# Kernel tuning notes

Hardware: AMD Instinct MI355X
Metric: run time of the kernel (lower is better)

The kernel has to match this reference:

```python
import jax, jax.numpy as jnp
import numpy as np

ROPE_BASE = 10000.0


def _apply_rope(q, k, start_pos):
    # q, k: (B, T, H, D) with half-split (LLaMA-style) rotation
    B, T, H, D = q.shape
    half = D // 2
    inv_freq = 1.0 / (ROPE_BASE ** (jnp.arange(0, half, dtype=jnp.float32) / half))
    pos = (start_pos + jnp.arange(T)).astype(jnp.float32)
    ang = pos[:, None] * inv_freq[None, :]          # (T, half)
    cos = jnp.cos(ang)[None, :, None, :]            # (1, T, 1, half)
    sin = jnp.sin(ang)[None, :, None, :]

    def rot(t):
        t1, t2 = t[..., :half], t[..., half:]
        return jnp.concatenate([t1 * cos - t2 * sin, t1 * sin + t2 * cos], axis=-1)

    return rot(q), rot(k)


def setup_inputs() -> dict:
    key = jax.random.key(0)
    k1, k2, k3 = jax.random.split(key, 3)
    B, T, C = 2, 2048, 2048
    x = jax.random.normal(k1, (B, T, C), dtype=jnp.float32)
    # torch Linear weights: (out_features, in_features), scaled like default init
    Wqkv = jax.random.normal(k2, (3 * C, C), dtype=jnp.float32) * (C ** -0.5)
    Wproj = jax.random.normal(k3, (C, C), dtype=jnp.float32) * (C ** -0.5)
    return {"x": x, "Wqkv": Wqkv, "Wproj": Wproj, "start_pos": 0}


def reference(x, Wqkv, Wproj, start_pos):
    B, T, C = x.shape
    H = 16
    D = C // H
    scale = D ** -0.5

    qkv = x @ Wqkv.T                                 # (B, T, 3C)
    q, k, v = jnp.split(qkv, 3, axis=-1)
    q = q.reshape(B, T, H, D)
    k = k.reshape(B, T, H, D)
    v = v.reshape(B, T, H, D)
    q, k = _apply_rope(q, k, start_pos)

    att = jnp.einsum("bthd,bshd->bhts", q, k) * scale   # (B, H, T, T)
    causal = jnp.tril(jnp.ones((T, T), dtype=bool))
    att = jnp.where(causal[None, None], att, -jnp.inf)
    att = jax.nn.softmax(att, axis=-1)
    out = jnp.einsum("bhts,bshd->bthd", att, v)          # (B, T, H, D)
    out = out.reshape(B, T, C)
    return out @ Wproj.T
```

## Files before the change

kernel.cpp:

```cpp
#include <hip/hip_runtime.h>
#include <hip/hip_bf16.h>
#include <stdint.h>
#include <math.h>

#define B_    2
#define T_    2048
#define C_    2048
#define H_    16
#define D_    128
#define NQKV  6144
#define BT_   4096

typedef __attribute__((ext_vector_type(8)))  short short8;
typedef __attribute__((ext_vector_type(4)))  short short4_;
typedef __attribute__((ext_vector_type(4)))  float float4_;
typedef __attribute__((ext_vector_type(16))) float f32x16;

__device__ __forceinline__ unsigned short f2bf(float f) {
  union { float f; unsigned int u; } v; v.f = f;
  unsigned int u = v.u;
  return (unsigned short)((u + 0x7FFFu + ((u >> 16) & 1u)) >> 16);
}
__device__ __forceinline__ float bf2f(unsigned short u) {
  union { unsigned int i; float f; } v; v.i = ((unsigned int)u) << 16;
  return v.f;
}
__device__ __forceinline__ void pk2(short4_& dst, int idx2, float a, float b) {
  union { __hip_bfloat162 h2; struct { short x, y; } s; } u;
  u.h2 = __float22bfloat162_rn(make_float2(a, b));
  dst[idx2 * 2]     = u.s.x;
  dst[idx2 * 2 + 1] = u.s.y;
}

__device__ __forceinline__ void async_cp16(const unsigned short* g, unsigned short* l) {
  __builtin_amdgcn_global_load_lds((__attribute__((address_space(1))) void*)g,
                                   (__attribute__((address_space(3))) void*)l,
                                   16, 0, 0);
}

__global__ __launch_bounds__(256) void cvt_all(const float* __restrict__ x,
                                               const float* __restrict__ wqkv,
                                               const float* __restrict__ wproj,
                                               const int* __restrict__ sp_ptr,
                                               unsigned short* __restrict__ out,
                                               float* __restrict__ ct,
                                               float* __restrict__ st) {
  if (blockIdx.x >= 12288) {
    int j = (blockIdx.x - 12288) * 256 + threadIdx.x;
    int d = j & 63;
    const float L2F = -0.20762050593046013f;
    float fr = exp2f((float)d * L2F);
    float ang = (float)(sp_ptr[0] + (j >> 6)) * fr;
    ct[j] = cosf(ang);
    st[j] = sinf(ang);
    return;
  }
  int i = (blockIdx.x * 256 + threadIdx.x) * 8;
  const float* src; int off;
  if (i < 8388608)       { src = x;     off = i; }
  else if (i < 20971520) { src = wqkv;  off = i - 8388608; }
  else                   { src = wproj; off = i - 20971520; }
  const float4_* p = (const float4_*)(src + off);
  float4_ a = p[0], b = p[1];
  short8 o;
  o[0] = (short)f2bf(a[0]); o[1] = (short)f2bf(a[1]);
  o[2] = (short)f2bf(a[2]); o[3] = (short)f2bf(a[3]);
  o[4] = (short)f2bf(b[0]); o[5] = (short)f2bf(b[1]);
  o[6] = (short)f2bf(b[2]); o[7] = (short)f2bf(b[3]);
  *(short8*)(out + i) = o;
}

template <bool F32OUT>
__global__ __launch_bounds__(256) void gemm_bt(const unsigned short* __restrict__ A,
                                               const unsigned short* __restrict__ Bm,
                                               void* __restrict__ Cout,
                                               int M, int N, int K) {
  __shared__ __align__(16) unsigned short As[128 * 64];
  __shared__ __align__(16) unsigned short Bs[128 * 64];
  const int tid  = threadIdx.x;
  const int lane = tid & 63;
  const int col16 = lane & 15, quad = lane >> 4;
  const int wave = tid >> 6;
  const int wm = wave >> 1, wn = wave & 1;
  const int m0 = blockIdx.y * 128, n0 = blockIdx.x * 128;

  float4_ acc[4][4] = {};

  #pragma unroll 1
  for (int k0 = 0; k0 < K; k0 += 64) {
    __syncthreads();
    #pragma unroll
    for (int i = 0; i < 4; ++i) {
      int P   = i * 256 + tid;
      int row = P >> 3;
      int kc  = (P & 7) ^ (row & 7);
      async_cp16(A  + (size_t)(m0 + row) * K + k0 + kc * 8, As + P * 8);
      async_cp16(Bm + (size_t)(n0 + row) * K + k0 + kc * 8, Bs + P * 8);
    }
    __syncthreads();
    #pragma unroll
    for (int ks = 0; ks < 2; ++ks) {
      short8 af[4], bf[4];
      #pragma unroll
      for (int i = 0; i < 4; ++i) {
        int ra = wm * 64 + i * 16 + col16;
        int ca = ((ks * 4 + quad) ^ (ra & 7)) * 8;
        af[i] = *(const short8*)(As + ra * 64 + ca);
        int rb = wn * 64 + i * 16 + col16;
        int cb = ((ks * 4 + quad) ^ (rb & 7)) * 8;
        bf[i] = *(const short8*)(Bs + rb * 64 + cb);
      }
      #pragma unroll
      for (int i = 0; i < 4; ++i)
        #pragma unroll
        for (int j = 0; j < 4; ++j)
          acc[i][j] = __builtin_amdgcn_mfma_f32_16x16x32_bf16(af[i], bf[j], acc[i][j], 0, 0, 0);
    }
  }

  #pragma unroll
  for (int i = 0; i < 4; ++i) {
    int mg = m0 + wm * 64 + i * 16 + quad * 4;
    #pragma unroll
    for (int j = 0; j < 4; ++j) {
      int ng = n0 + wn * 64 + j * 16 + col16;
      #pragma unroll
      for (int r = 0; r < 4; ++r) {
        if constexpr (F32OUT)
          ((float*)Cout)[(size_t)(mg + r) * N + ng] = acc[i][j][r];
        else
          ((unsigned short*)Cout)[(size_t)(mg + r) * N + ng] = f2bf(acc[i][j][r]);
      }
    }
  }
}

__global__ __launch_bounds__(256) void gemm_qkv(const unsigned short* __restrict__ A,
                                                const unsigned short* __restrict__ Bm,
                                                const float* __restrict__ ct,
                                                const float* __restrict__ st,
                                                unsigned short* __restrict__ q_r,
                                                unsigned short* __restrict__ k_r,
                                                unsigned short* __restrict__ v_t) {
  __shared__ __align__(16) unsigned short S[16384];
  unsigned short* As = S;
  unsigned short* Bs = S + 8192;
  const int tid  = threadIdx.x;
  const int lane = tid & 63;
  const int col16 = lane & 15, quad = lane >> 4;
  const int wave = tid >> 6;
  const int wm = wave >> 1, wn = wave & 1;
  const int m0 = blockIdx.y * 128, n0 = blockIdx.x * 128;

  float4_ acc[4][4] = {};

  #pragma unroll 1
  for (int k0 = 0; k0 < C_; k0 += 64) {
    __syncthreads();
    #pragma unroll
    for (int i = 0; i < 4; ++i) {
      int P   = i * 256 + tid;
      int row = P >> 3;
      int kc  = (P & 7) ^ (row & 7);
      async_cp16(A  + (size_t)(m0 + row) * C_ + k0 + kc * 8, As + P * 8);
      async_cp16(Bm + (size_t)(n0 + row) * C_ + k0 + kc * 8, Bs + P * 8);
    }
    __syncthreads();
    #pragma unroll
    for (int ks = 0; ks < 2; ++ks) {
      short8 af[4], bf[4];
      #pragma unroll
      for (int i = 0; i < 4; ++i) {
        int ra = wm * 64 + i * 16 + col16;
        int ca = ((ks * 4 + quad) ^ (ra & 7)) * 8;
        af[i] = *(const short8*)(As + ra * 64 + ca);
        int rb = wn * 32 + (i & 1) * 16 + (i >> 1) * 64 + col16;
        int cb = ((ks * 4 + quad) ^ (rb & 7)) * 8;
        bf[i] = *(const short8*)(Bs + rb * 64 + cb);
      }
      #pragma unroll
      for (int i = 0; i < 4; ++i)
        #pragma unroll
        for (int j = 0; j < 4; ++j)
          acc[i][j] = __builtin_amdgcn_mfma_f32_16x16x32_bf16(af[i], bf[j], acc[i][j], 0, 0, 0);
    }
  }

  const int region = n0 >> 11;
  const int h   = (n0 & 2047) >> 7;
  const int b   = m0 >> 11;
  const int t0l = m0 & 2047;
  const int bh  = b * H_ + h;

  if (region < 2) {
    unsigned short* dst = region ? k_r : q_r;
    const float scl = region ? 1.0f : 0.1275174117f;
    #pragma unroll
    for (int i = 0; i < 4; ++i) {
      int tl = t0l + wm * 64 + i * 16 + quad * 4;
      #pragma unroll
      for (int jl = 0; jl < 2; ++jl) {
        int d = wn * 32 + jl * 16 + col16;
        size_t ob = (size_t)(bh * T_ + tl) * D_ + d;
        int ti = tl * 64 + d;
        #pragma unroll
        for (int r = 0; r < 4; ++r) {
          float cs = ct[ti + r * 64], sn = st[ti + r * 64];
          float lo = acc[i][jl][r], hi = acc[i][jl + 2][r];
          dst[ob + (size_t)r * D_]      = f2bf((lo * cs - hi * sn) * scl);
          dst[ob + (size_t)r * D_ + 64] = f2bf((lo * sn + hi * cs) * scl);
        }
      }
    }
  } else {
    __syncthreads();
    #pragma unroll
    for (int i = 0; i < 4; ++i) {
      int tlb = wm * 64 + i * 16 + quad * 4;
      #pragma unroll
      for (int j = 0; j < 4; ++j) {
        int d = wn * 32 + (j & 1) * 16 + (j >> 1) * 64 + col16;
        #pragma unroll
        for (int r = 0; r < 4; ++r) {
          int t = tlb + r;
          int ch = (t >> 3) ^ (d & 15);
          S[d * 128 + ch * 8 + (t & 7)] = f2bf(acc[i][j][r]);
        }
      }
    }
    __syncthreads();
    int drow = tid >> 1, hf = tid & 1;
    size_t gb = (size_t)(bh * D_ + drow) * T_ + t0l + hf * 64;
    #pragma unroll
    for (int cc = 0; cc < 8; ++cc) {
      int ch = (hf * 8 + cc) ^ (drow & 15);
      *(short8*)(v_t + gb + cc * 8) = *(const short8*)(S + drow * 128 + ch * 8);
    }
  }
}

__global__ __launch_bounds__(256) void attn_fwd(const unsigned short* __restrict__ q_r,
                                                const unsigned short* __restrict__ k_r,
                                                const unsigned short* __restrict__ v_t,
                                                unsigned short* __restrict__ Ob) {
  __shared__ __align__(16) unsigned short Ks[2][64 * 128];
  __shared__ __align__(16) unsigned short Vts[2][128 * 64];
  __shared__ __align__(16) unsigned short Ps[128 * 64];
  const int g     = blockIdx.x >> 5;
  const int bh    = blockIdx.x & 31;
  const int qt    = (g < 8) ? g : 23 - g;
  const int tid  = threadIdx.x;
  const int lane = tid & 63;
  const int l31  = lane & 31;
  const int hi   = lane >> 5;
  const int w    = tid >> 6;
  const float NEG_INF = -__builtin_inff();
  const int b = bh >> 4, h = bh & 15;
  const int qlr = w * 32 + l31;

  const int q0 = qt * 128;
  const int njt = 2 * qt + 2;

  short8 qf[8];
  const unsigned short* qp = q_r + (size_t)(bh * T_ + q0 + qlr) * D_;
  #pragma unroll
  for (int ks = 0; ks < 8; ++ks) qf[ks] = *(const short8*)(qp + ks * 16 + hi * 8);

  f32x16 oacc[4] = {};
  float m_i = NEG_INF, l_i = 0.f;

  const unsigned short* kbase = k_r + (size_t)bh * T_ * D_;
  const unsigned short* vbase = v_t + (size_t)bh * D_ * T_;
  #define STAGE(JT, BUF)                                                        \
    {                                                                           \
      const unsigned short* kb = kbase + (size_t)(JT) * 64 * D_;                \
      const unsigned short* vb = vbase + (size_t)(JT) * 64;                     \
      unsigned short* kd = &Ks[(BUF)][0];                                       \
      unsigned short* vd = &Vts[(BUF)][0];                                      \
      _Pragma("unroll")                                                         \
      for (int i = 0; i < 4; ++i) {                                             \
        int P = i * 256 + tid;                                                  \
        int krow = P >> 4, kc = (P & 15) ^ (krow & 7);                          \
        async_cp16(kb + krow * D_ + kc * 8, kd + P * 8);                        \
        int vrow = P >> 3, vc = (P & 7) ^ (vrow & 7);                           \
        async_cp16(vb + (size_t)vrow * T_ + vc * 8, vd + P * 8);                \
      }                                                                         \
    }

  STAGE(0, 0);

  #pragma unroll 1
  for (int jt = 0; jt < njt; ++jt) {
    __syncthreads();
    if (jt + 1 < njt) STAGE(jt + 1, (jt + 1) & 1);

    if (jt * 64 > q0 + w * 32 + 31) continue;

    const unsigned short* KsB  = &Ks[jt & 1][0];
    const unsigned short* VtsB = &Vts[jt & 1][0];

    f32x16 s32[2];
    #pragma unroll
    for (int jn = 0; jn < 2; ++jn) {
      f32x16 a = {};
      #pragma unroll
      for (int ks = 0; ks < 8; ++ks) {
        int kr = jn * 32 + l31;
        int ch = ((ks * 2 + hi) ^ (kr & 7)) * 8;
        short8 kfr = *(const short8*)(KsB + kr * 128 + ch);
        a = __builtin_amdgcn_mfma_f32_32x32x16_bf16(kfr, qf[ks], a, 0, 0, 0);
      }
      s32[jn] = a;
    }
    if (jt * 64 + 63 > q0 + w * 32) {
      #pragma unroll
      for (int jn = 0; jn < 2; ++jn)
        #pragma unroll
        for (int reg = 0; reg < 16; ++reg) {
          int mrow = (reg & 3) + 8 * (reg >> 2) + 4 * hi;
          if (jt * 64 + jn * 32 + mrow > q0 + qlr) s32[jn][reg] = NEG_INF;
        }
    }
    float rm = NEG_INF;
    #pragma unroll
    for (int jn = 0; jn < 2; ++jn)
      #pragma unroll
      for (int reg = 0; reg < 16; ++reg) rm = fmaxf(rm, s32[jn][reg]);
    rm = fmaxf(rm, __shfl_xor(rm, 32));
    float m_new = fmaxf(m_i, rm);
    float alpha = exp2f(m_i - m_new);
    float rs = 0.f;
    #pragma unroll
    for (int jn = 0; jn < 2; ++jn)
      #pragma unroll
      for (int reg = 0; reg < 16; ++reg) {
        float pv = exp2f(s32[jn][reg] - m_new);
        s32[jn][reg] = pv;
        rs += pv;
      }
    rs += __shfl_xor(rs, 32);
    l_i = l_i * alpha + rs;
    m_i = m_new;
    #pragma unroll
    for (int dt = 0; dt < 4; ++dt) oacc[dt] *= alpha;

    #pragma unroll
    for (int jn = 0; jn < 2; ++jn)
      #pragma unroll
      for (int gg = 0; gg < 4; ++gg) {
        short4_ pkv;
        pk2(pkv, 0, s32[jn][gg * 4 + 0], s32[jn][gg * 4 + 1]);
        pk2(pkv, 1, s32[jn][gg * 4 + 2], s32[jn][gg * 4 + 3]);
        int chv = (jn * 4 + gg) ^ (qlr & 7);
        *(short4_*)(Ps + qlr * 64 + chv * 8 + hi * 4) = pkv;
      }
    __builtin_amdgcn_s_waitcnt(0xC07F);

    short8 pfv[4];
    #pragma unroll
    for (int ks2 = 0; ks2 < 4; ++ks2) {
      int ch = ((ks2 * 2 + hi) ^ (qlr & 7)) * 8;
      pfv[ks2] = *(const short8*)(Ps + qlr * 64 + ch);
    }
    #pragma unroll
    for (int dt = 0; dt < 4; ++dt)
      #pragma unroll
      for (int ks2 = 0; ks2 < 4; ++ks2) {
        int vr = dt * 32 + l31;
        int ch = ((ks2 * 2 + hi) ^ (vr & 7)) * 8;
        short8 vf = *(const short8*)(VtsB + vr * 64 + ch);
        oacc[dt] = __builtin_amdgcn_mfma_f32_32x32x16_bf16(vf, pfv[ks2], oacc[dt], 0, 0, 0);
      }
  }

  float inv_l = 1.0f / l_i;
  size_t ob = (size_t)(b * T_ + q0 + qlr) * C_ + h * D_;
  #pragma unroll
  for (int dt = 0; dt < 4; ++dt)
    #pragma unroll
    for (int gg = 0; gg < 4; ++gg) {
      int d = dt * 32 + 8 * gg + 4 * hi;
      short4_ o4;
      pk2(o4, 0, oacc[dt][gg * 4 + 0] * inv_l, oacc[dt][gg * 4 + 1] * inv_l);
      pk2(o4, 1, oacc[dt][gg * 4 + 2] * inv_l, oacc[dt][gg * 4 + 3] * inv_l);
      *(short4_*)(Ob + ob + d) = o4;
    }
  #undef STAGE
}

extern "C" void kernel_launch(void* const* d_in, const int* in_sizes, int n_in,
                              void* d_out, int out_size, void* d_ws, size_t ws_size,
                              hipStream_t stream) {
  const float* x     = (const float*)d_in[0];
  const float* Wqkv  = (const float*)d_in[1];
  const float* Wproj = (const float*)d_in[2];
  const int*   sp    = (const int*)d_in[3];
  float* out = (float*)d_out;

  unsigned short* ws     = (unsigned short*)d_ws;
  unsigned short* xb     = ws;
  unsigned short* wqkvb  = xb + 8388608;
  unsigned short* wprojb = wqkvb + 12582912;
  unsigned short* q_r    = wprojb + 4194304;
  unsigned short* k_r    = q_r + 8388608;
  unsigned short* v_t    = k_r + 8388608;
  float*          ctab   = (float*)(v_t + 8388608);
  float*          stab   = ctab + 131072;
  unsigned short* Obuf   = xb;

  cvt_all<<<12800, 256, 0, stream>>>(x, Wqkv, Wproj, sp, ws, ctab, stab);

  gemm_qkv<<<dim3(48, 32), 256, 0, stream>>>(xb, wqkvb, ctab, stab, q_r, k_r, v_t);

  attn_fwd<<<dim3(512), 256, 0, stream>>>(q_r, k_r, v_t, Obuf);

  gemm_bt<true><<<dim3(16, 32), 256, 0, stream>>>(Obuf, wprojb, (void*)out, BT_, C_, C_);
}
```

Before: 379.3 us.

## Skip online-softmax rescale under threshold and pass P via cross-lane shuffles

Adds a lazy rescaling rule to the flash-attention loop: the running max and the output/sum rescale update only when some lane's new row max exceeds the stored max by more than a threshold (log2 units), which removes most exp2 and oacc multiply work. It also drops the LDS round trip that turned the P tile into an MFMA operand. The bf16 P values are now exchanged between wave halves with __shfl_xor and rebuilt in registers. This frees the Ps shared buffer and its wait, at the cost of extra shuffles and the risk of larger exponent values when the max is not refreshed.

```diff
diff --git a/kernel.cpp b/kernel.cpp
--- a/kernel.cpp
+++ b/kernel.cpp
@@ -30,6 +30,12 @@
   u.h2 = __float22bfloat162_rn(make_float2(a, b));
   dst[idx2 * 2]     = u.s.x;
   dst[idx2 * 2 + 1] = u.s.y;
+}
+__device__ __forceinline__ short4_ shfl_xor32_s4(short4_ v) {
+  union { short4_ s; int i[2]; } u; u.s = v;
+  u.i[0] = __shfl_xor(u.i[0], 32);
+  u.i[1] = __shfl_xor(u.i[1], 32);
+  return u.s;
 }
 
 __device__ __forceinline__ void async_cp16(const unsigned short* g, unsigned short* l) {
@@ -245,7 +251,6 @@
                                                 unsigned short* __restrict__ Ob) {
   __shared__ __align__(16) unsigned short Ks[2][64 * 128];
   __shared__ __align__(16) unsigned short Vts[2][128 * 64];
-  __shared__ __align__(16) unsigned short Ps[128 * 64];
   const int g     = blockIdx.x >> 5;
   const int bh    = blockIdx.x & 31;
   const int qt    = (g < 8) ? g : 23 - g;
@@ -327,41 +332,47 @@
       #pragma unroll
       for (int reg = 0; reg < 16; ++reg) rm = fmaxf(rm, s32[jn][reg]);
     rm = fmaxf(rm, __shfl_xor(rm, 32));
-    float m_new = fmaxf(m_i, rm);
-    float alpha = exp2f(m_i - m_new);
+    if (!__all(rm <= m_i + 11.5f)) {
+      float m_new = fmaxf(m_i, rm);
+      float alpha = exp2f(m_i - m_new);
+      l_i *= alpha;
+      #pragma unroll
+      for (int dt = 0; dt < 4; ++dt) oacc[dt] *= alpha;
+      m_i = m_new;
+    }
     float rs = 0.f;
     #pragma unroll
     for (int jn = 0; jn < 2; ++jn)
       #pragma unroll
       for (int reg = 0; reg < 16; ++reg) {
-        float pv = exp2f(s32[jn][reg] - m_new);
+        float pv = exp2f(s32[jn][reg] - m_i);
         s32[jn][reg] = pv;
         rs += pv;
       }
     rs += __shfl_xor(rs, 32);
-    l_i = l_i * alpha + rs;
-    m_i = m_new;
-    #pragma unroll
-    for (int dt = 0; dt < 4; ++dt) oacc[dt] *= alpha;
-
-    #pragma unroll
-    for (int jn = 0; jn < 2; ++jn)
+    l_i += rs;
+
+    short8 pfv[4];
+    #pragma unroll
+    for (int jn = 0; jn < 2; ++jn) {
+      short4_ pk[4], ot[4];
       #pragma unroll
       for (int gg = 0; gg < 4; ++gg) {
-        short4_ pkv;
-        pk2(pkv, 0, s32[jn][gg * 4 + 0], s32[jn][gg * 4 + 1]);
-        pk2(pkv, 1, s32[jn][gg * 4 + 2], s32[jn][gg * 4 + 3]);
-        int chv = (jn * 4 + gg) ^ (qlr & 7);
-        *(short4_*)(Ps + qlr * 64 + chv * 8 + hi * 4) = pkv;
-      }
-    __builtin_amdgcn_s_waitcnt(0xC07F);
-
-    short8 pfv[4];
-    #pragma unroll
-    for (int ks2 = 0; ks2 < 4; ++ks2) {
-      int ch = ((ks2 * 2 + hi) ^ (qlr & 7)) * 8;
-      pfv[ks2] = *(const short8*)(Ps + qlr * 64 + ch);
-    }
+        pk2(pk[gg], 0, s32[jn][gg * 4 + 0], s32[jn][gg * 4 + 1]);
+        pk2(pk[gg], 1, s32[jn][gg * 4 + 2], s32[jn][gg * 4 + 3]);
+        ot[gg] = shfl_xor32_s4(pk[gg]);
+      }
+      #pragma unroll
+      for (int q = 0; q < 2; ++q) {
+        short4_ lo4 = hi ? ot[2 * q + 1] : pk[2 * q];
+        short4_ hi4 = hi ? pk[2 * q + 1] : ot[2 * q];
+        short8 bf_;
+        bf_[0] = lo4[0]; bf_[1] = lo4[1]; bf_[2] = lo4[2]; bf_[3] = lo4[3];
+        bf_[4] = hi4[0]; bf_[5] = hi4[1]; bf_[6] = hi4[2]; bf_[7] = hi4[3];
+        pfv[jn * 2 + q] = bf_;
+      }
+    }
+
     #pragma unroll
     for (int dt = 0; dt < 4; ++dt)
       #pragma unroll
```

Result: slower. 397.1 us (+4.7%).
